# Performance work log

Hardware: AMD Instinct MI355X
Metric: run time of the kernel (lower is better)

## Reference

```python
import jax, jax.numpy as jnp
import numpy as np

H, KVH, DH = 16, 4, 128
EPS = 1e-8

def _rmsnorm(t, gamma):
    # normalize over last dim (dim_head)
    ms = jnp.mean(t * t, axis=-1, keepdims=True)
    return t * jax.lax.rsqrt(ms + EPS) * gamma

def setup_inputs() -> dict:
    key = jax.random.key(0)
    ks = jax.random.split(key, 5)
    d = H * DH  # 2048
    kv_d = KVH * DH  # 512
    x = jax.random.normal(ks[0], (2, 2048, d), dtype=jnp.float32)
    Wq = jax.random.normal(ks[1], (d, d), dtype=jnp.float32) * (d ** -0.5)
    Wk = jax.random.normal(ks[2], (d, kv_d), dtype=jnp.float32) * (d ** -0.5)
    Wv = jax.random.normal(ks[3], (d, kv_d), dtype=jnp.float32) * (d ** -0.5)
    Wo = jax.random.normal(ks[4], (d, d), dtype=jnp.float32) * (d ** -0.5)
    q_gamma = jnp.ones((DH,), dtype=jnp.float32)
    k_gamma = jnp.ones((DH,), dtype=jnp.float32)
    return {"x": x, "Wq": Wq, "Wk": Wk, "Wv": Wv, "Wo": Wo,
            "q_gamma": q_gamma, "k_gamma": k_gamma}

def reference(x, Wq, Wk, Wv, Wo, q_gamma, k_gamma):
    b, s, d = x.shape
    g = H // KVH  # GQA group size
    q = (x @ Wq).reshape(b, s, H, DH)
    k = (x @ Wk).reshape(b, s, KVH, DH)
    v = (x @ Wv).reshape(b, s, KVH, DH)
    # fused QK RMSNorm (per-head, over dim_head)
    q = _rmsnorm(q, q_gamma)
    k = _rmsnorm(k, k_gamma)
    # GQA: expand kv heads across query-head groups
    k = jnp.repeat(k, g, axis=2)  # [b, s, H, DH]
    v = jnp.repeat(v, g, axis=2)
    scores = jnp.einsum('bqhd,bkhd->bhqk', q, k) * (DH ** -0.5)
    causal = jnp.tril(jnp.ones((s, s), dtype=bool))
    scores = jnp.where(causal, scores, jnp.finfo(scores.dtype).min)
    attn = jax.nn.softmax(scores, axis=-1)
    out = jnp.einsum('bhqk,bkhd->bqhd', attn, v).reshape(b, s, H * DH)
    out = out @ Wo
    return out + x  # residual skip
```

## Files before the change

### kernel.cpp

```cpp
#include <hip/hip_runtime.h>

typedef unsigned short u16;
typedef __attribute__((ext_vector_type(8))) short short8;
typedef __attribute__((ext_vector_type(4))) float f32x4;

#define DEVI __device__ __forceinline__

DEVI float u2f(u16 u) {
    unsigned int x = ((unsigned int)u) << 16;
    float f; __builtin_memcpy(&f, &x, 4); return f;
}
DEVI u16 f2u(float f) {
    unsigned int x; __builtin_memcpy(&x, &f, 4);
    x = (x + 0x7fffu + ((x >> 16) & 1u)) >> 16;
    return (u16)x;
}
DEVI unsigned int fbits(float f) {
    unsigned int x; __builtin_memcpy(&x, &f, 4); return x;
}
DEVI void gld16(const u16* g, u16* ldsbase) {
    __builtin_amdgcn_global_load_lds(
        (const __attribute__((address_space(1))) unsigned int*)g,
        (__attribute__((address_space(3))) unsigned int*)ldsbase, 16, 0, 0);
}

__global__ __launch_bounds__(256) void prep(
    const float* __restrict__ x,
    const float* __restrict__ Wq, const float* __restrict__ Wk,
    const float* __restrict__ Wv, const float* __restrict__ Wo,
    u16* __restrict__ xbf, u16* __restrict__ WTqkv, u16* __restrict__ WoT)
{
    __shared__ u16 T[64 * 72];
    int id = blockIdx.x;
    const int tid = threadIdx.x;
    if (id < 4096) {
        int g = (id * 256 + tid) * 8;
        float4 a = *(const float4*)&x[g];
        float4 c = *(const float4*)&x[g + 4];
        short8 v;
        v[0]=(short)f2u(a.x); v[1]=(short)f2u(a.y); v[2]=(short)f2u(a.z); v[3]=(short)f2u(a.w);
        v[4]=(short)f2u(c.x); v[5]=(short)f2u(c.y); v[6]=(short)f2u(c.z); v[7]=(short)f2u(c.w);
        *(short8*)&xbf[g] = v;
        return;
    }
    id -= 4096;
    const float* W; u16* WT; int N, bx, by;
    if (id < 1024)      {            W = Wo; WT = WoT;   N = 2048; bx = id & 31; by = id >> 5; }
    else if (id < 2048) { id -= 1024; W = Wq; WT = WTqkv; N = 2048; bx = id & 31; by = id >> 5; }
    else if (id < 2304) { id -= 2048; W = Wk; WT = WTqkv + (size_t)2048 * 2048; N = 512; bx = id & 7; by = id >> 3; }
    else                { id -= 2304; W = Wv; WT = WTqkv + (size_t)2560 * 2048; N = 512; bx = id & 7; by = id >> 3; }
    const int K = 2048;
    const int k0 = by * 64, n0 = bx * 64;
#pragma unroll
    for (int i = 0; i < 2; ++i) {
        int c = tid + i * 256;
        int row = c >> 3, n8 = (c & 7) * 8;
        const float* src = &W[(size_t)(k0 + row) * N + n0 + n8];
#pragma unroll
        for (int j = 0; j < 8; ++j)
            T[(n8 + j) * 72 + row] = f2u(src[j]);
    }
    __syncthreads();
#pragma unroll
    for (int i = 0; i < 2; ++i) {
        int c = tid + i * 256;
        int n = c >> 3, k8 = (c & 7) * 8;
        *(short8*)&WT[(size_t)(n0 + n) * K + k0 + k8] = *(const short8*)&T[n * 72 + k8];
    }
}

__global__ __launch_bounds__(256) void gemm_lds(
    const u16* __restrict__ A, int lda,
    const u16* __restrict__ WT,
    void* __restrict__ C, int ldc, const float* __restrict__ resid, int c_f32,
    int M, int N, int K,
    const float* __restrict__ qg, const float* __restrict__ kg, int fuse_norm)
{
    __shared__ u16 As[128 * 32];
    __shared__ u16 Bs[128 * 32];
    const int tid = threadIdx.x;
    const int lane = tid & 63, w = tid >> 6;
    const int wm = w >> 1, wn = w & 1;
    const int l15 = lane & 15, quad = lane >> 4;
    const int r4 = lane >> 2, c4 = (lane & 3) * 8;
    const int m0 = blockIdx.y * 128, n0 = blockIdx.x * 128;

    f32x4 acc[4][4] = {};
    for (int k0 = 0; k0 < K; k0 += 32) {
#pragma unroll
        for (int j = 0; j < 2; ++j) {
            int row = w * 32 + j * 16;
            gld16(&WT[(size_t)(n0 + row + r4) * K + k0 + c4], &Bs[row * 32]);
            gld16(&A [(size_t)(m0 + row + r4) * lda + k0 + c4], &As[row * 32]);
        }
        __syncthreads();
        short8 a[4], b[4];
#pragma unroll
        for (int mt = 0; mt < 4; ++mt)
            a[mt] = *(const short8*)&As[(wm * 64 + mt * 16 + l15) * 32 + quad * 8];
#pragma unroll
        for (int nt = 0; nt < 4; ++nt)
            b[nt] = *(const short8*)&Bs[(wn * 64 + nt * 16 + l15) * 32 + quad * 8];
#pragma unroll
        for (int mt = 0; mt < 4; ++mt)
#pragma unroll
            for (int nt = 0; nt < 4; ++nt)
                acc[mt][nt] = __builtin_amdgcn_mfma_f32_16x16x32_bf16(a[mt], b[nt], acc[mt][nt], 0, 0, 0);
        __syncthreads();
    }

    if (fuse_norm && n0 < 2560) {
        const float* gamma = (n0 < 2048) ? qg : kg;
        float* red = (float*)As;
#pragma unroll
        for (int mt = 0; mt < 4; ++mt)
#pragma unroll
            for (int r = 0; r < 4; ++r) {
                float p = 0.f;
#pragma unroll
                for (int nt = 0; nt < 4; ++nt) p += acc[mt][nt][r] * acc[mt][nt][r];
#pragma unroll
                for (int msk = 1; msk < 16; msk <<= 1) p += __shfl_xor(p, msk);
                if (l15 == 0)
                    red[(wm * 64 + mt * 16 + quad * 4 + r) * 2 + wn] = p;
            }
        __syncthreads();
        float gv[4];
#pragma unroll
        for (int nt = 0; nt < 4; ++nt) gv[nt] = gamma[wn * 64 + nt * 16 + l15];
#pragma unroll
        for (int mt = 0; mt < 4; ++mt)
#pragma unroll
            for (int r = 0; r < 4; ++r) {
                int rl = wm * 64 + mt * 16 + quad * 4 + r;
                float m2 = red[rl * 2] + red[rl * 2 + 1];
                float sc = rsqrtf(m2 * (1.0f / 128.0f) + 1e-8f);
#pragma unroll
                for (int nt = 0; nt < 4; ++nt) acc[mt][nt][r] *= sc * gv[nt];
            }
    }

#pragma unroll
    for (int mt = 0; mt < 4; ++mt) {
#pragma unroll
        for (int r = 0; r < 4; ++r) {
            int row = m0 + wm * 64 + mt * 16 + quad * 4 + r;
#pragma unroll
            for (int nt = 0; nt < 4; ++nt) {
                int col = n0 + wn * 64 + nt * 16 + l15;
                float v = acc[mt][nt][r];
                if (resid) v += resid[(size_t)row * ldc + col];
                if (c_f32) ((float*)C)[(size_t)row * ldc + col] = v;
                else       ((u16*)C)[(size_t)row * ldc + col] = f2u(v);
            }
        }
    }
}

__global__ __launch_bounds__(256) void vtrans(
    const u16* __restrict__ qkv, u16* __restrict__ vT)
{
    __shared__ u16 T[128 * 72];
    const int tid = threadIdx.x;
    const int t0 = blockIdx.x * 64;
    const int kvh = blockIdx.y, b = blockIdx.z;
#pragma unroll
    for (int i = 0; i < 4; ++i) {
        int c = tid + i * 256;
        int tl = c >> 4, d8 = (c & 15) * 8;
        short8 v = *(const short8*)&qkv[(size_t)(b * 2048 + t0 + tl) * 3072 + 2560 + kvh * 128 + d8];
#pragma unroll
        for (int j = 0; j < 8; ++j)
            T[(d8 + j) * 72 + tl] = (u16)v[j];
    }
    __syncthreads();
#pragma unroll
    for (int i = 0; i < 4; ++i) {
        int c = tid + i * 256;
        int d = c >> 3, t8 = (c & 7) * 8;
        *(short8*)&vT[((size_t)(b * 4 + kvh) * 128 + d) * 2048 + t0 + t8] =
            *(const short8*)&T[d * 72 + t8];
    }
}

#define QS 136
#define VS 72
__global__ __launch_bounds__(512) void attn(
    u16* __restrict__ qkv, const u16* __restrict__ vT)
{
    __shared__ u16 lds[17920];
    u16* const Ks = lds;
    u16* const Vs = lds + 8704;

    const int tid = threadIdx.x, lane = tid & 63, w = tid >> 6;
    const int t = w >> 2, wq = w & 3;
    const int l15 = lane & 15, quad = lane >> 4;
    const int h = blockIdx.y, b = blockIdx.z;
    const int kvh = h >> 2;
    const int qts[2] = { (int)blockIdx.x, 31 - (int)blockIdx.x };
    const int qt = qts[t];
    const float scale = 0.08838834764831845f;

#pragma unroll
    for (int ts = 0; ts < 2; ++ts)
#pragma unroll
        for (int i = 0; i < 2; ++i) {
            int c = tid + i * 512;
            int r = c >> 4, d8 = (c & 15) * 8;
            *(short8*)&lds[ts * 8704 + r * QS + d8] =
                *(const short8*)&qkv[(size_t)(b * 2048 + qts[ts] * 64 + r) * 3072 + h * 128 + d8];
        }
    __syncthreads();
    short8 qf[4];
#pragma unroll
    for (int ks = 0; ks < 4; ++ks)
        qf[ks] = *(const short8*)&lds[t * 8704 + (wq * 16 + l15) * QS + ks * 32 + quad * 8];
    __syncthreads();

    f32x4 o[8] = {};
    float m_ = -1e30f, l_ = 0.f;

    for (int kt = 0; kt <= qts[1]; ++kt) {
        const int kv0 = kt * 64;
#pragma unroll
        for (int i = 0; i < 2; ++i) {
            int c = tid + i * 512;
            int r = c >> 4, d8 = (c & 15) * 8;
            *(short8*)&Ks[r * QS + d8] =
                *(const short8*)&qkv[(size_t)(b * 2048 + kv0 + r) * 3072 + 2048 + kvh * 128 + d8];
        }
#pragma unroll
        for (int i = 0; i < 2; ++i) {
            int c = tid + i * 512;
            int d = c >> 3, t8 = (c & 7) * 8;
            *(short8*)&Vs[d * VS + t8] =
                *(const short8*)&vT[((size_t)(b * 4 + kvh) * 128 + d) * 2048 + kv0 + t8];
        }
        __syncthreads();

        if (kt <= qt) {
            f32x4 s[4];
#pragma unroll
            for (int nt = 0; nt < 4; ++nt) {
                f32x4 a = {};
#pragma unroll
                for (int ks = 0; ks < 4; ++ks) {
                    short8 kf = *(const short8*)&Ks[(nt * 16 + l15) * QS + ks * 32 + quad * 8];
                    a = __builtin_amdgcn_mfma_f32_16x16x32_bf16(kf, qf[ks], a, 0, 0, 0);
                }
                s[nt] = a;
            }
            if (kt == qt) {
                int qrow = wq * 16 + l15;
#pragma unroll
                for (int nt = 0; nt < 4; ++nt)
#pragma unroll
                    for (int r = 0; r < 4; ++r) {
                        float v = s[nt][r] * scale;
                        if (nt * 16 + quad * 4 + r > qrow) v = -1e30f;
                        s[nt][r] = v;
                    }
            } else {
#pragma unroll
                for (int nt = 0; nt < 4; ++nt)
#pragma unroll
                    for (int r = 0; r < 4; ++r) s[nt][r] *= scale;
            }
            float mx = s[0][0];
#pragma unroll
            for (int nt = 0; nt < 4; ++nt)
#pragma unroll
                for (int r = 0; r < 4; ++r) mx = fmaxf(mx, s[nt][r]);
            mx = fmaxf(mx, __shfl_xor(mx, 16));
            mx = fmaxf(mx, __shfl_xor(mx, 32));
            float mn = fmaxf(m_, mx);
            float alpha = __expf(m_ - mn);
            m_ = mn;
            float sum = 0.f;
#pragma unroll
            for (int nt = 0; nt < 4; ++nt)
#pragma unroll
                for (int r = 0; r < 4; ++r) {
                    float p = __expf(s[nt][r] - mn);
                    s[nt][r] = p;
                    sum += p;
                }
            sum += __shfl_xor(sum, 16);
            sum += __shfl_xor(sum, 32);
            l_ = l_ * alpha + sum;
            unsigned int pk[4][2];
#pragma unroll
            for (int nt = 0; nt < 4; ++nt)
#pragma unroll
                for (int i = 0; i < 2; ++i)
                    pk[nt][i] = __builtin_amdgcn_perm(
                        fbits(s[nt][2 * i + 1]), fbits(s[nt][2 * i]), 0x07060302u);
            int af[2][4];
#pragma unroll
            for (int c = 0; c < 2; ++c)
#pragma unroll
                for (int d = 0; d < 4; ++d) {
                    int src = l15 + 16 * ((quad & 1) * 2 + (d >> 1));
                    int v0 = __shfl((int)pk[2 * c][d & 1], src);
                    int v1 = __shfl((int)pk[2 * c + 1][d & 1], src);
                    af[c][d] = (quad >= 2) ? v1 : v0;
                }
            union { int i4[4]; short8 s8; } ua0, ua1;
#pragma unroll
            for (int d = 0; d < 4; ++d) { ua0.i4[d] = af[0][d]; ua1.i4[d] = af[1][d]; }
#pragma unroll
            for (int r = 0; r < 4; ++r) {
                float ao = __shfl(alpha, quad * 4 + r);
#pragma unroll
                for (int nto = 0; nto < 8; ++nto) o[nto][r] *= ao;
            }
#pragma unroll
            for (int nto = 0; nto < 8; ++nto) {
                short8 bv0 = *(const short8*)&Vs[(nto * 16 + l15) * VS + quad * 8];
                short8 bv1 = *(const short8*)&Vs[(nto * 16 + l15) * VS + 32 + quad * 8];
                o[nto] = __builtin_amdgcn_mfma_f32_16x16x32_bf16(ua0.s8, bv0, o[nto], 0, 0, 0);
                o[nto] = __builtin_amdgcn_mfma_f32_16x16x32_bf16(ua1.s8, bv1, o[nto], 0, 0, 0);
            }
        }
        __syncthreads();
    }
    {
        float rl = 1.0f / l_;
#pragma unroll
        for (int r = 0; r < 4; ++r) {
            float inv = __shfl(rl, quad * 4 + r);
            int row = qt * 64 + wq * 16 + quad * 4 + r;
#pragma unroll
            for (int nto = 0; nto < 8; ++nto)
                qkv[(size_t)(b * 2048 + row) * 3072 + h * 128 + nto * 16 + l15] =
                    f2u(o[nto][r] * inv);
        }
    }
}

extern "C" void kernel_launch(void* const* d_in, const int* in_sizes, int n_in,
                              void* d_out, int out_size, void* d_ws, size_t ws_size,
                              hipStream_t stream) {
    const float* x  = (const float*)d_in[0];
    const float* Wq = (const float*)d_in[1];
    const float* Wk = (const float*)d_in[2];
    const float* Wv = (const float*)d_in[3];
    const float* Wo = (const float*)d_in[4];
    const float* qg = (const float*)d_in[5];
    const float* kg = (const float*)d_in[6];

    char* ws = (char*)d_ws;
    u16* WoT   = (u16*)(ws);
    u16* QKV   = (u16*)(ws + 8388608);
    u16* vT    = (u16*)(ws + 33554432);
    u16* WTqkv = (u16*)(ws + 33554432);
    u16* xbf   = (u16*)d_out;

    prep<<<dim3(6656), 256, 0, stream>>>(x, Wq, Wk, Wv, Wo, xbf, WTqkv, WoT);

    gemm_lds<<<dim3(24, 32), 256, 0, stream>>>(xbf, 2048, WTqkv, QKV, 3072,
                                               nullptr, 0, 4096, 3072, 2048,
                                               qg, kg, 1);

    vtrans<<<dim3(32, 4, 2), 256, 0, stream>>>(QKV, vT);

    attn<<<dim3(16, 16, 2), 512, 0, stream>>>(QKV, vT);

    gemm_lds<<<dim3(16, 32), 256, 0, stream>>>(QKV, 3072, WoT, d_out, 2048,
                                               x, 1, 4096, 2048, 2048,
                                               nullptr, nullptr, 0);
}
```

Baseline: 370.6 us.

## Drop LDS staging in attention and load Q/K/V fragments directly from global

```diff
diff --git a/kernel.cpp b/kernel.cpp
--- a/kernel.cpp
+++ b/kernel.cpp
@@ -183,15 +183,9 @@
     }
 }
 
-#define QS 136
-#define VS 72
 __global__ __launch_bounds__(512) void attn(
     u16* __restrict__ qkv, const u16* __restrict__ vT)
 {
-    __shared__ u16 lds[17920];
-    u16* const Ks = lds;
-    u16* const Vs = lds + 8704;
-
     const int tid = threadIdx.x, lane = tid & 63, w = tid >> 6;
     const int t = w >> 2, wq = w & 3;
     const int l15 = lane & 15, quad = lane >> 4;
@@ -201,128 +195,102 @@
     const int qt = qts[t];
     const float scale = 0.08838834764831845f;
 
-#pragma unroll
-    for (int ts = 0; ts < 2; ++ts)
-#pragma unroll
-        for (int i = 0; i < 2; ++i) {
-            int c = tid + i * 512;
-            int r = c >> 4, d8 = (c & 15) * 8;
-            *(short8*)&lds[ts * 8704 + r * QS + d8] =
-                *(const short8*)&qkv[(size_t)(b * 2048 + qts[ts] * 64 + r) * 3072 + h * 128 + d8];
-        }
-    __syncthreads();
+    const u16* const Qg = &qkv[(size_t)(b * 2048 + qt * 64 + wq * 16 + l15) * 3072 + h * 128 + quad * 8];
+    const u16* const Kg = &qkv[(size_t)(b * 2048 + l15) * 3072 + 2048 + kvh * 128 + quad * 8];
+    const u16* const Vg = &vT[((size_t)(b * 4 + kvh) * 128 + l15) * 2048 + quad * 8];
+
     short8 qf[4];
 #pragma unroll
     for (int ks = 0; ks < 4; ++ks)
-        qf[ks] = *(const short8*)&lds[t * 8704 + (wq * 16 + l15) * QS + ks * 32 + quad * 8];
-    __syncthreads();
+        qf[ks] = *(const short8*)&Qg[ks * 32];
 
     f32x4 o[8] = {};
     float m_ = -1e30f, l_ = 0.f;
 
-    for (int kt = 0; kt <= qts[1]; ++kt) {
+    for (int kt = 0; kt <= qt; ++kt) {
         const int kv0 = kt * 64;
-#pragma unroll
-        for (int i = 0; i < 2; ++i) {
-            int c = tid + i * 512;
-            int r = c >> 4, d8 = (c & 15) * 8;
-            *(short8*)&Ks[r * QS + d8] =
-                *(const short8*)&qkv[(size_t)(b * 2048 + kv0 + r) * 3072 + 2048 + kvh * 128 + d8];
-        }
-#pragma unroll
-        for (int i = 0; i < 2; ++i) {
-            int c = tid + i * 512;
-            int d = c >> 3, t8 = (c & 7) * 8;
-            *(short8*)&Vs[d * VS + t8] =
-                *(const short8*)&vT[((size_t)(b * 4 + kvh) * 128 + d) * 2048 + kv0 + t8];
-        }
-        __syncthreads();
-
-        if (kt <= qt) {
-            f32x4 s[4];
-#pragma unroll
-            for (int nt = 0; nt < 4; ++nt) {
-                f32x4 a = {};
-#pragma unroll
-                for (int ks = 0; ks < 4; ++ks) {
-                    short8 kf = *(const short8*)&Ks[(nt * 16 + l15) * QS + ks * 32 + quad * 8];
-                    a = __builtin_amdgcn_mfma_f32_16x16x32_bf16(kf, qf[ks], a, 0, 0, 0);
+        f32x4 s[4];
+#pragma unroll
+        for (int nt = 0; nt < 4; ++nt) {
+            f32x4 a = {};
+#pragma unroll
+            for (int ks = 0; ks < 4; ++ks) {
+                short8 kf = *(const short8*)&Kg[(size_t)(kv0 + nt * 16) * 3072 + ks * 32];
+                a = __builtin_amdgcn_mfma_f32_16x16x32_bf16(kf, qf[ks], a, 0, 0, 0);
+            }
+            s[nt] = a;
+        }
+        if (kt == qt) {
+            int qrow = wq * 16 + l15;
+#pragma unroll
+            for (int nt = 0; nt < 4; ++nt)
+#pragma unroll
+                for (int r = 0; r < 4; ++r) {
+                    float v = s[nt][r] * scale;
+                    if (nt * 16 + quad * 4 + r > qrow) v = -1e30f;
+                    s[nt][r] = v;
                 }
-                s[nt] = a;
-            }
-            if (kt == qt) {
-                int qrow = wq * 16 + l15;
-#pragma unroll
-                for (int nt = 0; nt < 4; ++nt)
-#pragma unroll
-                    for (int r = 0; r < 4; ++r) {
-                        float v = s[nt][r] * scale;
-                        if (nt * 16 + quad * 4 + r > qrow) v = -1e30f;
-                        s[nt][r] = v;
-                    }
-            } else {
-#pragma unroll
-                for (int nt = 0; nt < 4; ++nt)
-#pragma unroll
-                    for (int r = 0; r < 4; ++r) s[nt][r] *= scale;
-            }
-            float mx = s[0][0];
+        } else {
 #pragma unroll
             for (int nt = 0; nt < 4; ++nt)
 #pragma unroll
-                for (int r = 0; r < 4; ++r) mx = fmaxf(mx, s[nt][r]);
-            mx = fmaxf(mx, __shfl_xor(mx, 16));
-            mx = fmaxf(mx, __shfl_xor(mx, 32));
-            float mn = fmaxf(m_, mx);
-            float alpha = __expf(m_ - mn);
-            m_ = mn;
-            float sum = 0.f;
-#pragma unroll
-            for (int nt = 0; nt < 4; ++nt)
-#pragma unroll
-                for (int r = 0; r < 4; ++r) {
-                    float p = __expf(s[nt][r] - mn);
-                    s[nt][r] = p;
-                    sum += p;
-                }
-            sum += __shfl_xor(sum, 16);
-            sum += __shfl_xor(sum, 32);
-            l_ = l_ * alpha + sum;
-            unsigned int pk[4][2];
-#pragma unroll
-            for (int nt = 0; nt < 4; ++nt)
-#pragma unroll
-                for (int i = 0; i < 2; ++i)
-                    pk[nt][i] = __builtin_amdgcn_perm(
-                        fbits(s[nt][2 * i + 1]), fbits(s[nt][2 * i]), 0x07060302u);
-            int af[2][4];
-#pragma unroll
-            for (int c = 0; c < 2; ++c)
-#pragma unroll
-                for (int d = 0; d < 4; ++d) {
-                    int src = l15 + 16 * ((quad & 1) * 2 + (d >> 1));
-                    int v0 = __shfl((int)pk[2 * c][d & 1], src);
-                    int v1 = __shfl((int)pk[2 * c + 1][d & 1], src);
-                    af[c][d] = (quad >= 2) ? v1 : v0;
-                }
-            union { int i4[4]; short8 s8; } ua0, ua1;
-#pragma unroll
-            for (int d = 0; d < 4; ++d) { ua0.i4[d] = af[0][d]; ua1.i4[d] = af[1][d]; }
+                for (int r = 0; r < 4; ++r) s[nt][r] *= scale;
+        }
+        float mx = s[0][0];
+#pragma unroll
+        for (int nt = 0; nt < 4; ++nt)
+#pragma unroll
+            for (int r = 0; r < 4; ++r) mx = fmaxf(mx, s[nt][r]);
+        mx = fmaxf(mx, __shfl_xor(mx, 16));
+        mx = fmaxf(mx, __shfl_xor(mx, 32));
+        float mn = fmaxf(m_, mx);
+        float alpha = __expf(m_ - mn);
+        m_ = mn;
+        float sum = 0.f;
+#pragma unroll
+        for (int nt = 0; nt < 4; ++nt)
 #pragma unroll
             for (int r = 0; r < 4; ++r) {
-                float ao = __shfl(alpha, quad * 4 + r);
-#pragma unroll
-                for (int nto = 0; nto < 8; ++nto) o[nto][r] *= ao;
-            }
-#pragma unroll
-            for (int nto = 0; nto < 8; ++nto) {
-                short8 bv0 = *(const short8*)&Vs[(nto * 16 + l15) * VS + quad * 8];
-                short8 bv1 = *(const short8*)&Vs[(nto * 16 + l15) * VS + 32 + quad * 8];
-                o[nto] = __builtin_amdgcn_mfma_f32_16x16x32_bf16(ua0.s8, bv0, o[nto], 0, 0, 0);
-                o[nto] = __builtin_amdgcn_mfma_f32_16x16x32_bf16(ua1.s8, bv1, o[nto], 0, 0, 0);
-            }
-        }
-        __syncthreads();
+                float p = __expf(s[nt][r] - mn);
+                s[nt][r] = p;
+                sum += p;
+            }
+        sum += __shfl_xor(sum, 16);
+        sum += __shfl_xor(sum, 32);
+        l_ = l_ * alpha + sum;
+        unsigned int pk[4][2];
+#pragma unroll
+        for (int nt = 0; nt < 4; ++nt)
+#pragma unroll
+            for (int i = 0; i < 2; ++i)
+                pk[nt][i] = __builtin_amdgcn_perm(
+                    fbits(s[nt][2 * i + 1]), fbits(s[nt][2 * i]), 0x07060302u);
+        int af[2][4];
+#pragma unroll
+        for (int c = 0; c < 2; ++c)
+#pragma unroll
+            for (int d = 0; d < 4; ++d) {
+                int src = l15 + 16 * ((quad & 1) * 2 + (d >> 1));
+                int v0 = __shfl((int)pk[2 * c][d & 1], src);
+                int v1 = __shfl((int)pk[2 * c + 1][d & 1], src);
+                af[c][d] = (quad >= 2) ? v1 : v0;
+            }
+        union { int i4[4]; short8 s8; } ua0, ua1;
+#pragma unroll
+        for (int d = 0; d < 4; ++d) { ua0.i4[d] = af[0][d]; ua1.i4[d] = af[1][d]; }
+#pragma unroll
+        for (int r = 0; r < 4; ++r) {
+            float ao = __shfl(alpha, quad * 4 + r);
+#pragma unroll
+            for (int nto = 0; nto < 8; ++nto) o[nto][r] *= ao;
+        }
+#pragma unroll
+        for (int nto = 0; nto < 8; ++nto) {
+            short8 bv0 = *(const short8*)&Vg[(size_t)(nto * 16) * 2048 + kv0];
+            short8 bv1 = *(const short8*)&Vg[(size_t)(nto * 16) * 2048 + kv0 + 32];
+            o[nto] = __builtin_amdgcn_mfma_f32_16x16x32_bf16(ua0.s8, bv0, o[nto], 0, 0, 0);
+            o[nto] = __builtin_amdgcn_mfma_f32_16x16x32_bf16(ua1.s8, bv1, o[nto], 0, 0, 0);
+        }
     }
     {
         float rl = 1.0f / l_;
```

Result: slower. 575.2 us (+55.2%).
